# Performance work log

Measured on AMD Instinct MI355X. Metric: run time of the kernel, lower is better.

The kernel has to match this reference:

```python
import jax, jax.numpy as jnp
import numpy as np

B, S, D = 4, 2048, 512
H = 8
DK = D // H
DFF = 2048
EPS = 1e-5


def _layernorm(x, g, b):
    mu = jnp.mean(x, axis=-1, keepdims=True)
    var = jnp.mean((x - mu) ** 2, axis=-1, keepdims=True)
    return (x - mu) * jax.lax.rsqrt(var + EPS) * g + b


def setup_inputs() -> dict:
    key = jax.random.key(0)
    ks = jax.random.split(key, 12)
    s = 1.0 / np.sqrt(D)
    sf = 1.0 / np.sqrt(DFF)
    return {
        "x": jax.random.normal(ks[0], (B, S, D), dtype=jnp.float32),
        "Wq": jax.random.uniform(ks[1], (D, D), jnp.float32, -s, s),
        "bq": jnp.zeros((D,), jnp.float32),
        "Wk": jax.random.uniform(ks[2], (D, D), jnp.float32, -s, s),
        "bk": jnp.zeros((D,), jnp.float32),
        "Wv": jax.random.uniform(ks[3], (D, D), jnp.float32, -s, s),
        "bv": jnp.zeros((D,), jnp.float32),
        "Wo": jax.random.uniform(ks[4], (D, D), jnp.float32, -s, s),
        "bo": jnp.zeros((D,), jnp.float32),
        "W1": jax.random.uniform(ks[5], (D, DFF), jnp.float32, -s, s),
        "b1": jnp.zeros((DFF,), jnp.float32),
        "W2": jax.random.uniform(ks[6], (DFF, D), jnp.float32, -sf, sf),
        "b2": jnp.zeros((D,), jnp.float32),
        "g1": jnp.ones((D,), jnp.float32),
        "be1": jnp.zeros((D,), jnp.float32),
        "g2": jnp.ones((D,), jnp.float32),
        "be2": jnp.zeros((D,), jnp.float32),
    }


def reference(x, Wq, bq, Wk, bk, Wv, bv, Wo, bo, W1, b1, W2, b2, g1, be1, g2, be2):
    # Multi-head attention (dropout = identity at eval)
    def heads(v):  # [B,S,D] -> [B,H,S,DK]
        return v.reshape(B, S, H, DK).transpose(0, 2, 1, 3)

    q = heads(x @ Wq + bq)
    k = heads(x @ Wk + bk)
    v = heads(x @ Wv + bv)
    scores = jnp.einsum("bhsd,bhtd->bhst", q, k) / np.sqrt(DK)
    attn = jax.nn.softmax(scores, axis=-1)
    ctx = jnp.einsum("bhst,bhtd->bhsd", attn, v)
    ctx = ctx.transpose(0, 2, 1, 3).reshape(B, S, D)
    attn_out = ctx @ Wo + bo

    x1 = _layernorm(x + attn_out, g1, be1)

    ff = jax.nn.relu(x1 @ W1 + b1) @ W2 + b2
    return _layernorm(x1 + ff, g2, be2)
```

## Files before the change

kernel.cpp:

```cpp
#include <hip/hip_runtime.h>
#include <hip/hip_bf16.h>
#include <stdint.h>

typedef __bf16 bf16;
typedef __attribute__((ext_vector_type(8))) __bf16 bf16x8;
typedef __attribute__((ext_vector_type(4))) float f32x4;

#define DEVI __device__ __forceinline__

constexpr int Bz = 4, Sz = 2048, Dz = 512, Hz = 8, DKz = 64, DFFz = 2048;
constexpr int ROWSz = Bz * Sz;
constexpr float EPSf = 1e-5f;
constexpr float C2f = 0.125f * 1.44269504088896f;

DEVI void load_lds16(void* lds, const void* g) {
  __builtin_amdgcn_global_load_lds(
      (const __attribute__((address_space(1))) void*)(uintptr_t)(g),
      (__attribute__((address_space(3))) void*)(uint32_t)(uintptr_t)(lds),
      16, 0, 0);
}

DEVI void permswap32(unsigned& x, unsigned& y) {
  asm("v_permlane32_swap_b32 %0, %1" : "+v"(x), "+v"(y));
}
DEVI void permswap16(unsigned& x, unsigned& y) {
  asm("v_permlane16_swap_b32 %0, %1" : "+v"(x), "+v"(y));
}

template <int BM, int BK, int EPI>
__global__ __launch_bounds__(256, BM == 128 ? 4 : 3) void gemm_bt(
    const bf16* __restrict__ A, const bf16* __restrict__ Bt,
    const float* __restrict__ bias, const float* __restrict__ resid,
    const bf16* __restrict__ residb, bf16* __restrict__ aux,
    void* __restrict__ Cout, int M, int N, int K) {
  constexpr int BN = 128;
  constexpr int MI = BM / 32;
  constexpr int RPI = 512 / BK;
  constexpr int AISS = (BM / 4) / RPI;
  constexpr int BISS = 32 / RPI;
  __shared__ alignas(16) bf16 sA[2][BM * BK];
  __shared__ alignas(16) bf16 sB[2][BN * BK];
  const int tid = threadIdx.x;
  const int lane = tid & 63;
  const int wv = tid >> 6;
  const int n0 = blockIdx.x * BN;
  const int m0 = blockIdx.y * BM;

  const int srow = (BK == 32) ? (lane >> 2) : (lane >> 3);
  const int sch = (BK == 32) ? (((lane & 3) ^ (srow & 3)) * 8)
                             : (((lane & 7) ^ (srow & 7)) * 8);
  const bf16* gA = A + (size_t)(m0 + wv * (BM / 4) + srow) * K + sch;
  const bf16* gB = Bt + (size_t)(n0 + wv * 32 + srow) * K + sch;

  const int wm = (wv >> 1) * (BM / 2);
  const int wn = (wv & 1) * 64;
  const int fr = lane & 15;
  const int fq = lane >> 4;

  auto stage = [&](int buf, int k0) {
#pragma unroll
    for (int j = 0; j < AISS; ++j)
      load_lds16(sA[buf] + (wv * (BM / 4) + j * RPI) * BK, gA + (size_t)(j * RPI) * K + k0);
#pragma unroll
    for (int j = 0; j < BISS; ++j)
      load_lds16(sB[buf] + (wv * 32 + j * RPI) * BK, gB + (size_t)(j * RPI) * K + k0);
  };

  f32x4 acc[MI][4] = {};

  stage(0, 0);
  __syncthreads();

  const int niter = K / BK;
  for (int it = 0; it < niter; ++it) {
    const int cur = it & 1;
    if (it + 1 < niter) stage(cur ^ 1, (it + 1) * BK);
#pragma unroll
    for (int kk = 0; kk < BK / 32; ++kk) {
      const int fc = (BK == 32) ? ((fq ^ (fr & 3)) * 8)
                                : (((4 * kk + fq) ^ (fr & 7)) * 8);
      bf16x8 af[MI], bfr[4];
#pragma unroll
      for (int i = 0; i < MI; ++i)
        af[i] = *(const bf16x8*)(sA[cur] + (wm + i * 16 + fr) * BK + fc);
#pragma unroll
      for (int j = 0; j < 4; ++j)
        bfr[j] = *(const bf16x8*)(sB[cur] + (wn + j * 16 + fr) * BK + fc);
#pragma unroll
      for (int i = 0; i < MI; ++i)
#pragma unroll
        for (int j = 0; j < 4; ++j)
          acc[i][j] = __builtin_amdgcn_mfma_f32_16x16x32_bf16(af[i], bfr[j], acc[i][j], 0, 0, 0);
    }
    __syncthreads();
  }

#pragma unroll
  for (int i = 0; i < MI; ++i) {
#pragma unroll
    for (int j = 0; j < 4; ++j) {
      const int col = n0 + wn + j * 16 + fr;
      const float bv = bias[col];
      if (EPI == 3 && col >= 1024) {
        const int row0 = m0 + wm + i * 16 + fq * 4;
        const int hh = (col - 1024) >> 6, dk = (col - 1024) & 63;
        const int bb = row0 >> 11, s0 = row0 & 2047;
        bf16 pv[4];
#pragma unroll
        for (int r = 0; r < 4; ++r) pv[r] = (bf16)(acc[i][j][r] + bv);
        *(uint2*)(aux + (size_t)((bb * 8 + hh) * 64 + dk) * 2048 + s0) = *(const uint2*)pv;
      } else {
#pragma unroll
        for (int r = 0; r < 4; ++r) {
          const int row = m0 + wm + i * 16 + fq * 4 + r;
          const size_t idx = (size_t)row * N + col;
          float v = acc[i][j][r] + bv;
          if (EPI == 1) {
            ((bf16*)Cout)[idx] = (bf16)(v + resid[idx]);
          } else if (EPI == 2) {
            ((bf16*)Cout)[idx] = (bf16)(v > 0.f ? v : 0.f);
          } else if (EPI == 3) {
            ((bf16*)Cout)[idx] = (bf16)(col < 512 ? v * C2f : v);
          } else {
            ((bf16*)Cout)[idx] = (bf16)(v + (float)residb[idx]);
          }
        }
      }
    }
  }
}

__global__ __launch_bounds__(256, 2) void flash_attn(
    const bf16* __restrict__ qkv, const bf16* __restrict__ Vt,
    bf16* __restrict__ ctx) {
  const int bid = blockIdx.x;
  const int qt = bid & 15;
  const int h = (bid >> 4) & 7;
  const int b = bid >> 7;
  const int q0 = qt * 128;
  const int tid = threadIdx.x, lane = tid & 63, wv = tid >> 6;
  const int fr = lane & 15, fq = lane >> 4;
  const int xsw = fr & 7;

  __shared__ alignas(16) bf16 sK[3][64 * 64];
  __shared__ alignas(16) bf16 sV[3][64 * 64];

  const int srow = lane >> 3;
  const int scol = ((lane & 7) ^ srow) * 8;

  const bf16* gQ = qkv + (size_t)(b * Sz + q0 + wv * 32 + srow) * 1536 + h * 64 + scol;
  const bf16* gK = qkv + (size_t)(b * Sz + wv * 16 + srow) * 1536 + 512 + h * 64 + scol;
  const bf16* gV = Vt + (size_t)((b * 8 + h) * 64 + wv * 16 + srow) * Sz + scol;

  bf16* sQ = (bf16*)sK;
#pragma unroll
  for (int i = 0; i < 4; ++i)
    load_lds16(sQ + (wv * 32 + i * 8) * 64, gQ + (size_t)(i * 8) * 1536);
  asm volatile("s_waitcnt vmcnt(0)" ::: "memory");

  const int colc0 = (fq ^ xsw) * 8;
  const int colc1 = ((fq + 4) ^ xsw) * 8;
  int qsrc[4];
#pragma unroll
  for (int r = 0; r < 4; ++r) qsrc[r] = (fq * 4 + r) | (lane & 48);

  bf16x8 qb[2][2];
#pragma unroll
  for (int s = 0; s < 2; ++s) {
    qb[s][0] = *(const bf16x8*)(sQ + (wv * 32 + s * 16 + fr) * 64 + colc0);
    qb[s][1] = *(const bf16x8*)(sQ + (wv * 32 + s * 16 + fr) * 64 + colc1);
  }
  asm volatile("s_waitcnt lgkmcnt(0)" ::: "memory");
  __syncthreads();

  auto stage = [&](int buf, int t) {
    const size_t t0r = (size_t)t * 64;
    load_lds16(sK[buf] + (wv * 16 + 0) * 64, gK + t0r * 1536);
    load_lds16(sK[buf] + (wv * 16 + 8) * 64, gK + (t0r + 8) * 1536);
    load_lds16(sV[buf] + (wv * 16 + 0) * 64, gV + t0r);
    load_lds16(sV[buf] + (wv * 16 + 8) * 64, gV + (size_t)8 * Sz + t0r);
  };

  stage(0, 0);
  stage(1, 1);
  asm volatile("s_waitcnt vmcnt(4)" ::: "memory");
  __builtin_amdgcn_s_barrier();
  asm volatile("" ::: "memory");

  float l_part[2] = {0.f, 0.f};
  f32x4 acc_o[2][4] = {};
  int cur = 0;

  for (int it = 0; it < 32; ++it) {
    if (it + 2 < 32) {
      int nb = cur + 2;
      if (nb >= 3) nb -= 3;
      stage(nb, it + 2);
    }

    bf16x8 kf[2][4];
#pragma unroll
    for (int j = 0; j < 4; ++j) {
      kf[0][j] = *(const bf16x8*)(sK[cur] + (j * 16 + fr) * 64 + colc0);
      kf[1][j] = *(const bf16x8*)(sK[cur] + (j * 16 + fr) * 64 + colc1);
    }
    f32x4 sc[2][4] = {};
    __builtin_amdgcn_s_setprio(1);
#pragma unroll
    for (int s = 0; s < 2; ++s)
#pragma unroll
      for (int kk = 0; kk < 2; ++kk)
#pragma unroll
        for (int j = 0; j < 4; ++j)
          sc[s][j] = __builtin_amdgcn_mfma_f32_16x16x32_bf16(kf[kk][j], qb[s][kk], sc[s][j], 0, 0, 0);
    __builtin_amdgcn_s_setprio(0);

    bf16x8 pa[2][2];
#pragma unroll
    for (int s = 0; s < 2; ++s) {
      unsigned c0[4], c1[4];
      float rs = 0.f;
#pragma unroll
      for (int j = 0; j < 4; ++j) {
        float e0 = __builtin_amdgcn_exp2f(sc[s][j][0]);
        float e1 = __builtin_amdgcn_exp2f(sc[s][j][1]);
        float e2 = __builtin_amdgcn_exp2f(sc[s][j][2]);
        float e3 = __builtin_amdgcn_exp2f(sc[s][j][3]);
        rs += (e0 + e1) + (e2 + e3);
        union { bf16 hh[2]; unsigned u; } pka, pkb;
        pka.hh[0] = (bf16)e0; pka.hh[1] = (bf16)e1;
        pkb.hh[0] = (bf16)e2; pkb.hh[1] = (bf16)e3;
        c0[j] = pka.u;
        c1[j] = pkb.u;
      }
      l_part[s] += rs;
#pragma unroll
      for (int kk = 0; kk < 2; ++kk) {
        unsigned x0 = c0[2 * kk], y0 = c0[2 * kk + 1];
        permswap32(x0, y0);
        permswap16(x0, y0);
        unsigned x1 = c1[2 * kk], y1 = c1[2 * kk + 1];
        permswap32(x1, y1);
        permswap16(x1, y1);
        union { unsigned u[4]; bf16x8 v; } pk;
        pk.u[0] = x0; pk.u[1] = x1; pk.u[2] = y0; pk.u[3] = y1;
        pa[s][kk] = pk.v;
      }
    }

    bf16x8 vf[2][4];
#pragma unroll
    for (int j = 0; j < 4; ++j) {
      vf[0][j] = *(const bf16x8*)(sV[cur] + (j * 16 + fr) * 64 + colc0);
      vf[1][j] = *(const bf16x8*)(sV[cur] + (j * 16 + fr) * 64 + colc1);
    }
    __builtin_amdgcn_s_setprio(1);
#pragma unroll
    for (int s = 0; s < 2; ++s)
#pragma unroll
      for (int kk = 0; kk < 2; ++kk)
#pragma unroll
        for (int j = 0; j < 4; ++j)
          acc_o[s][j] = __builtin_amdgcn_mfma_f32_16x16x32_bf16(pa[s][kk], vf[kk][j], acc_o[s][j], 0, 0, 0);
    __builtin_amdgcn_s_setprio(0);

    if (it < 31) {
      if (it < 30) asm volatile("s_waitcnt vmcnt(4)" ::: "memory");
      else         asm volatile("s_waitcnt vmcnt(0)" ::: "memory");
      __builtin_amdgcn_s_barrier();
      asm volatile("" ::: "memory");
    }
    cur = cur == 2 ? 0 : cur + 1;
  }

#pragma unroll
  for (int s = 0; s < 2; ++s) {
    float l = l_part[s];
    l += __shfl_xor(l, 16, 64);
    l += __shfl_xor(l, 32, 64);
    float rl[4];
#pragma unroll
    for (int r = 0; r < 4; ++r) rl[r] = 1.0f / __shfl(l, qsrc[r], 64);
#pragma unroll
    for (int j = 0; j < 4; ++j)
#pragma unroll
      for (int r = 0; r < 4; ++r) {
        const int row = b * Sz + q0 + wv * 32 + s * 16 + fq * 4 + r;
        const int col = h * 64 + j * 16 + fr;
        ctx[(size_t)row * Dz + col] = (bf16)(acc_o[s][j][r] * rl[r]);
      }
  }
}

template <int OUT_F32>
__global__ __launch_bounds__(256) void layer_norm_k(
    const bf16* __restrict__ y, const float* __restrict__ g,
    const float* __restrict__ be, void* __restrict__ out) {
  const int row = blockIdx.x * 4 + (threadIdx.x >> 6);
  const int lane = threadIdx.x & 63;
  const int col = lane * 8;
  bf16x8 hv = *(const bf16x8*)(y + (size_t)row * Dz + col);
  float v[8];
  float s = 0.f, ss = 0.f;
#pragma unroll
  for (int i = 0; i < 8; ++i) {
    v[i] = (float)hv[i];
    s += v[i];
    ss += v[i] * v[i];
  }
#pragma unroll
  for (int o = 1; o < 64; o <<= 1) {
    s += __shfl_xor(s, o, 64);
    ss += __shfl_xor(ss, o, 64);
  }
  const float mu = s * (1.0f / Dz);
  const float rstd = rsqrtf(ss * (1.0f / Dz) - mu * mu + EPSf);
  const float4* g4 = (const float4*)(g + col);
  const float4* b4 = (const float4*)(be + col);
  float4 ga = g4[0], gb = g4[1], ba = b4[0], bb = b4[1];
  float o8[8];
  o8[0] = (v[0] - mu) * rstd * ga.x + ba.x;
  o8[1] = (v[1] - mu) * rstd * ga.y + ba.y;
  o8[2] = (v[2] - mu) * rstd * ga.z + ba.z;
  o8[3] = (v[3] - mu) * rstd * ga.w + ba.w;
  o8[4] = (v[4] - mu) * rstd * gb.x + bb.x;
  o8[5] = (v[5] - mu) * rstd * gb.y + bb.y;
  o8[6] = (v[6] - mu) * rstd * gb.z + bb.z;
  o8[7] = (v[7] - mu) * rstd * gb.w + bb.w;
  if (OUT_F32) {
    float4* of = (float4*)((float*)out + (size_t)row * Dz + col);
    of[0] = make_float4(o8[0], o8[1], o8[2], o8[3]);
    of[1] = make_float4(o8[4], o8[5], o8[6], o8[7]);
  } else {
    bf16 ob[8];
#pragma unroll
    for (int i = 0; i < 8; ++i) ob[i] = (bf16)o8[i];
    *(uint4*)((bf16*)out + (size_t)row * Dz + col) = *(const uint4*)ob;
  }
}

__global__ __launch_bounds__(256) void prep_all(
    const float* __restrict__ Wq, const float* __restrict__ Wk,
    const float* __restrict__ Wv, const float* __restrict__ Wo,
    const float* __restrict__ W1, const float* __restrict__ W2,
    const float* __restrict__ bq, const float* __restrict__ bk,
    const float* __restrict__ bv, const float* __restrict__ x,
    bf16* __restrict__ WqkvT, bf16* __restrict__ WoT,
    bf16* __restrict__ W1T, bf16* __restrict__ W2T,
    float* __restrict__ bqkv, bf16* __restrict__ xb) {
  __shared__ float tile[64][65];
  const int blk = blockIdx.x;
  const int t = threadIdx.x;
  if (blk < 768) {
    const float* W;
    bf16* Wt;
    int K, N, local;
    if (blk < 64)       { W = Wq; Wt = WqkvT;                       K = 512;  N = 512;  local = blk; }
    else if (blk < 128) { W = Wk; Wt = WqkvT + (size_t)512 * 512;   K = 512;  N = 512;  local = blk - 64; }
    else if (blk < 192) { W = Wv; Wt = WqkvT + (size_t)1024 * 512;  K = 512;  N = 512;  local = blk - 128; }
    else if (blk < 256) { W = Wo; Wt = WoT;                         K = 512;  N = 512;  local = blk - 192; }
    else if (blk < 512) { W = W1; Wt = W1T;                         K = 512;  N = 2048; local = blk - 256; }
    else                { W = W2; Wt = W2T;                         K = 2048; N = 512;  local = blk - 512; }
    const int kt = K / 64;
    const int k0 = (local % kt) * 64, n0 = (local / kt) * 64;
    const int r = t >> 2, c = (t & 3) * 16;
    const float* src = W + (size_t)(k0 + r) * N + n0 + c;
#pragma unroll
    for (int i = 0; i < 4; ++i) {
      float4 v = ((const float4*)src)[i];
      tile[r][c + i * 4 + 0] = v.x;
      tile[r][c + i * 4 + 1] = v.y;
      tile[r][c + i * 4 + 2] = v.z;
      tile[r][c + i * 4 + 3] = v.w;
    }
    __syncthreads();
    union { bf16 hh[16]; uint4 u[2]; } pk;
#pragma unroll
    for (int i = 0; i < 16; ++i) pk.hh[i] = (bf16)tile[c + i][r];
    uint4* dst = (uint4*)(Wt + (size_t)(n0 + r) * K + k0 + c);
    dst[0] = pk.u[0];
    dst[1] = pk.u[1];
  } else if (blk == 768) {
    for (int i = t; i < 1536; i += 256)
      bqkv[i] = i < 512 ? bq[i] : (i < 1024 ? bk[i - 512] : bv[i - 1024]);
  } else {
    const int local = blk - 769;
#pragma unroll
    for (int k = 0; k < 4; ++k) {
      const int i = local * 1024 + k * 256 + t;
      float4 v = ((const float4*)x)[i];
      bf16 tv[4] = {(bf16)v.x, (bf16)v.y, (bf16)v.z, (bf16)v.w};
      ((uint2*)xb)[i] = *(const uint2*)tv;
    }
  }
}

extern "C" void kernel_launch(void* const* d_in, const int* in_sizes, int n_in,
                              void* d_out, int out_size, void* d_ws, size_t ws_size,
                              hipStream_t stream) {
  const float* x   = (const float*)d_in[0];
  const float* Wq  = (const float*)d_in[1];
  const float* bq  = (const float*)d_in[2];
  const float* Wk  = (const float*)d_in[3];
  const float* bk  = (const float*)d_in[4];
  const float* Wv  = (const float*)d_in[5];
  const float* bvp = (const float*)d_in[6];
  const float* Wo  = (const float*)d_in[7];
  const float* bo  = (const float*)d_in[8];
  const float* W1  = (const float*)d_in[9];
  const float* b1  = (const float*)d_in[10];
  const float* W2  = (const float*)d_in[11];
  const float* b2  = (const float*)d_in[12];
  const float* g1  = (const float*)d_in[13];
  const float* be1 = (const float*)d_in[14];
  const float* g2  = (const float*)d_in[15];
  const float* be2 = (const float*)d_in[16];

  char* ws = (char*)d_ws;
  size_t off = 0;
  auto alloc = [&](size_t bytes) -> void* {
    void* p = ws + off;
    off += (bytes + 255) & ~(size_t)255;
    return p;
  };
  bf16*  WqkvT = (bf16*)alloc((size_t)1536 * 512 * 2);
  float* bqkv  = (float*)alloc(1536 * 4);
  bf16*  WoT   = (bf16*)alloc((size_t)512 * 512 * 2);
  bf16*  W1T   = (bf16*)alloc((size_t)2048 * 512 * 2);
  bf16*  W2T   = (bf16*)alloc((size_t)512 * 2048 * 2);
  bf16*  xb    = (bf16*)alloc((size_t)ROWSz * 512 * 2);
  bf16*  qkv   = (bf16*)alloc((size_t)ROWSz * 1536 * 2);
  bf16*  Vt    = (bf16*)alloc((size_t)32 * 64 * 2048 * 2);
  bf16*  ctx   = (bf16*)alloc((size_t)ROWSz * 512 * 2);
  bf16*  y1    = (bf16*)alloc((size_t)ROWSz * 512 * 2);
  bf16*  x1b   = (bf16*)alloc((size_t)ROWSz * 512 * 2);
  bf16*  hbuf  = qkv;
  bf16*  y2    = y1;

  prep_all<<<dim3(1793), 256, 0, stream>>>(Wq, Wk, Wv, Wo, W1, W2, bq, bk, bvp, x,
                                           WqkvT, WoT, W1T, W2T, bqkv, xb);

  gemm_bt<128, 32, 3><<<dim3(12, 64), 256, 0, stream>>>(xb, WqkvT, bqkv, nullptr, nullptr, Vt, qkv, ROWSz, 1536, 512);
  flash_attn<<<dim3(512), 256, 0, stream>>>(qkv, Vt, ctx);
  gemm_bt<64, 64, 4><<<dim3(4, 128), 256, 0, stream>>>(ctx, WoT, bo, nullptr, xb, nullptr, y1, ROWSz, 512, 512);
  layer_norm_k<0><<<dim3(2048), 256, 0, stream>>>(y1, g1, be1, x1b);
  gemm_bt<128, 32, 2><<<dim3(16, 64), 256, 0, stream>>>(x1b, W1T, b1, nullptr, nullptr, nullptr, hbuf, ROWSz, 2048, 512);
  gemm_bt<64, 64, 4><<<dim3(4, 128), 256, 0, stream>>>(hbuf, W2T, b2, nullptr, x1b, nullptr, y2, ROWSz, 512, 2048);
  layer_norm_k<1><<<dim3(2048), 256, 0, stream>>>(y2, g2, be2, d_out);
}
```

Measured before the change: 251.0 us.

## Software-pipeline flash attention: overlap next-tile QK^T with current softmax and PV

Moves the attention loop to a four-buffer LDS ring with three tiles prefetched ahead instead of a three-buffer ring with two. The loop is restructured so each step computes scores for tile t+1 while exponentiating and multiplying scores for tile t, ping-ponging between two score register sets. The point is to keep the matrix units busy while exp and permute work runs, and to hide more global-load latency. In exchange it raises LDS use to 64KB per block and adds register pressure from the extra score set, which could limit occupancy at two blocks per CU.

Measured after the change: 243.9 us. 2.8% less time.

```diff
diff --git a/kernel.cpp b/kernel.cpp
--- a/kernel.cpp
+++ b/kernel.cpp
@@ -142,8 +142,8 @@
   const int fr = lane & 15, fq = lane >> 4;
   const int xsw = fr & 7;
 
-  __shared__ alignas(16) bf16 sK[3][64 * 64];
-  __shared__ alignas(16) bf16 sV[3][64 * 64];
+  __shared__ alignas(16) bf16 sK[4][64 * 64];
+  __shared__ alignas(16) bf16 sV[4][64 * 64];
 
   const int srow = lane >> 3;
   const int scol = ((lane & 7) ^ srow) * 8;
@@ -183,77 +183,98 @@
 
   stage(0, 0);
   stage(1, 1);
+  stage(2, 2);
+  asm volatile("s_waitcnt vmcnt(8)" ::: "memory");
+  __builtin_amdgcn_s_barrier();
+  asm volatile("" ::: "memory");
+
+  float l_part[2] = {0.f, 0.f};
+  f32x4 acc_o[2][4] = {};
+  f32x4 scA[2][4], scB[2][4];
+
+  {
+    bf16x8 kf[2][4];
+#pragma unroll
+    for (int j = 0; j < 4; ++j) {
+      kf[0][j] = *(const bf16x8*)(sK[0] + (j * 16 + fr) * 64 + colc0);
+      kf[1][j] = *(const bf16x8*)(sK[0] + (j * 16 + fr) * 64 + colc1);
+    }
+#pragma unroll
+    for (int s = 0; s < 2; ++s)
+#pragma unroll
+      for (int j = 0; j < 4; ++j) {
+        f32x4 z = {0.f, 0.f, 0.f, 0.f};
+        z = __builtin_amdgcn_mfma_f32_16x16x32_bf16(kf[0][j], qb[s][0], z, 0, 0, 0);
+        scA[s][j] = __builtin_amdgcn_mfma_f32_16x16x32_bf16(kf[1][j], qb[s][1], z, 0, 0, 0);
+      }
+  }
   asm volatile("s_waitcnt vmcnt(4)" ::: "memory");
   __builtin_amdgcn_s_barrier();
   asm volatile("" ::: "memory");
 
-  float l_part[2] = {0.f, 0.f};
-  f32x4 acc_o[2][4] = {};
-  int cur = 0;
-
-  for (int it = 0; it < 32; ++it) {
-    if (it + 2 < 32) {
-      int nb = cur + 2;
-      if (nb >= 3) nb -= 3;
-      stage(nb, it + 2);
-    }
-
-    bf16x8 kf[2][4];
+  auto body = [&](int t, f32x4 (&scC)[2][4], f32x4 (&scN)[2][4],
+                  bool do_stage, bool do_qkt, bool wait4, bool wait0, bool do_bar) {
+    if (do_stage) stage((t + 3) & 3, t + 3);
+
+    const bf16* kb = sK[(t + 1) & 3];
+    const bf16* vb = sV[t & 3];
+    bf16x8 kf[2][4], vf[2][4];
+    if (do_qkt) {
+#pragma unroll
+      for (int j = 0; j < 4; ++j) {
+        kf[0][j] = *(const bf16x8*)(kb + (j * 16 + fr) * 64 + colc0);
+        kf[1][j] = *(const bf16x8*)(kb + (j * 16 + fr) * 64 + colc1);
+      }
+    }
 #pragma unroll
     for (int j = 0; j < 4; ++j) {
-      kf[0][j] = *(const bf16x8*)(sK[cur] + (j * 16 + fr) * 64 + colc0);
-      kf[1][j] = *(const bf16x8*)(sK[cur] + (j * 16 + fr) * 64 + colc1);
-    }
-    f32x4 sc[2][4] = {};
+      vf[0][j] = *(const bf16x8*)(vb + (j * 16 + fr) * 64 + colc0);
+      vf[1][j] = *(const bf16x8*)(vb + (j * 16 + fr) * 64 + colc1);
+    }
+
+    unsigned c0[2][4], c1[2][4];
+    float rs0 = 0.f, rs1 = 0.f;
     __builtin_amdgcn_s_setprio(1);
 #pragma unroll
+    for (int g = 0; g < 8; ++g) {
+      const int s = g >> 2, j = g & 3;
+      if (do_qkt) {
+        f32x4 z = {0.f, 0.f, 0.f, 0.f};
+        z = __builtin_amdgcn_mfma_f32_16x16x32_bf16(kf[0][j], qb[s][0], z, 0, 0, 0);
+        scN[s][j] = __builtin_amdgcn_mfma_f32_16x16x32_bf16(kf[1][j], qb[s][1], z, 0, 0, 0);
+      }
+      float e0 = __builtin_amdgcn_exp2f(scC[s][j][0]);
+      float e1 = __builtin_amdgcn_exp2f(scC[s][j][1]);
+      float e2 = __builtin_amdgcn_exp2f(scC[s][j][2]);
+      float e3 = __builtin_amdgcn_exp2f(scC[s][j][3]);
+      if (s == 0) rs0 += (e0 + e1) + (e2 + e3);
+      else        rs1 += (e0 + e1) + (e2 + e3);
+      union { bf16 hh[2]; unsigned u; } pka, pkb;
+      pka.hh[0] = (bf16)e0; pka.hh[1] = (bf16)e1;
+      pkb.hh[0] = (bf16)e2; pkb.hh[1] = (bf16)e3;
+      c0[s][j] = pka.u;
+      c1[s][j] = pkb.u;
+    }
+    __builtin_amdgcn_s_setprio(0);
+    l_part[0] += rs0;
+    l_part[1] += rs1;
+
+    bf16x8 pa[2][2];
+#pragma unroll
     for (int s = 0; s < 2; ++s)
 #pragma unroll
-      for (int kk = 0; kk < 2; ++kk)
-#pragma unroll
-        for (int j = 0; j < 4; ++j)
-          sc[s][j] = __builtin_amdgcn_mfma_f32_16x16x32_bf16(kf[kk][j], qb[s][kk], sc[s][j], 0, 0, 0);
-    __builtin_amdgcn_s_setprio(0);
-
-    bf16x8 pa[2][2];
-#pragma unroll
-    for (int s = 0; s < 2; ++s) {
-      unsigned c0[4], c1[4];
-      float rs = 0.f;
-#pragma unroll
-      for (int j = 0; j < 4; ++j) {
-        float e0 = __builtin_amdgcn_exp2f(sc[s][j][0]);
-        float e1 = __builtin_amdgcn_exp2f(sc[s][j][1]);
-        float e2 = __builtin_amdgcn_exp2f(sc[s][j][2]);
-        float e3 = __builtin_amdgcn_exp2f(sc[s][j][3]);
-        rs += (e0 + e1) + (e2 + e3);
-        union { bf16 hh[2]; unsigned u; } pka, pkb;
-        pka.hh[0] = (bf16)e0; pka.hh[1] = (bf16)e1;
-        pkb.hh[0] = (bf16)e2; pkb.hh[1] = (bf16)e3;
-        c0[j] = pka.u;
-        c1[j] = pkb.u;
-      }
-      l_part[s] += rs;
-#pragma unroll
       for (int kk = 0; kk < 2; ++kk) {
-        unsigned x0 = c0[2 * kk], y0 = c0[2 * kk + 1];
+        unsigned x0 = c0[s][2 * kk], y0 = c0[s][2 * kk + 1];
         permswap32(x0, y0);
         permswap16(x0, y0);
-        unsigned x1 = c1[2 * kk], y1 = c1[2 * kk + 1];
+        unsigned x1 = c1[s][2 * kk], y1 = c1[s][2 * kk + 1];
         permswap32(x1, y1);
         permswap16(x1, y1);
         union { unsigned u[4]; bf16x8 v; } pk;
         pk.u[0] = x0; pk.u[1] = x1; pk.u[2] = y0; pk.u[3] = y1;
         pa[s][kk] = pk.v;
       }
-    }
-
-    bf16x8 vf[2][4];
-#pragma unroll
-    for (int j = 0; j < 4; ++j) {
-      vf[0][j] = *(const bf16x8*)(sV[cur] + (j * 16 + fr) * 64 + colc0);
-      vf[1][j] = *(const bf16x8*)(sV[cur] + (j * 16 + fr) * 64 + colc1);
-    }
+
     __builtin_amdgcn_s_setprio(1);
 #pragma unroll
     for (int s = 0; s < 2; ++s)
@@ -264,14 +285,22 @@
           acc_o[s][j] = __builtin_amdgcn_mfma_f32_16x16x32_bf16(pa[s][kk], vf[kk][j], acc_o[s][j], 0, 0, 0);
     __builtin_amdgcn_s_setprio(0);
 
-    if (it < 31) {
-      if (it < 30) asm volatile("s_waitcnt vmcnt(4)" ::: "memory");
-      else         asm volatile("s_waitcnt vmcnt(0)" ::: "memory");
+    if (wait4) asm volatile("s_waitcnt vmcnt(4)" ::: "memory");
+    if (wait0) asm volatile("s_waitcnt vmcnt(0)" ::: "memory");
+    if (do_bar) {
       __builtin_amdgcn_s_barrier();
       asm volatile("" ::: "memory");
     }
-    cur = cur == 2 ? 0 : cur + 1;
-  }
+  };
+
+  for (int t = 0; t < 28; t += 2) {
+    body(t,     scA, scB, true, true, true, false, true);
+    body(t + 1, scB, scA, true, true, true, false, true);
+  }
+  body(28, scA, scB, true,  true,  true,  false, true);
+  body(29, scB, scA, false, true,  false, true,  true);
+  body(30, scA, scB, false, true,  false, false, false);
+  body(31, scB, scA, false, false, false, false, false);
 
 #pragma unroll
   for (int s = 0; s < 2; ++s) {
```

## Shrink attention query tile to 64 rows and raise occupancy with double buffering

Applied to the files above, without the earlier changes.

The flash attention kernel now gives each block 64 query rows instead of 128, with each wave owning one 16-row slice. The grid doubles to 1024 blocks, and the launch bound rises to 4 blocks per CU. K/V staging drops from a triple buffer to a double buffer to save LDS, and Q is staged through a spare V buffer. The aim is more resident waves to hide latency and a better spread of blocks across CUs. The cost is halved K/V reuse per block, which doubles K/V global traffic, plus less load/compute overlap because of the full vmcnt(0) wait each iteration.

Result: faster. 245.8 us (-2.1%).

```diff
diff --git a/kernel.cpp b/kernel.cpp
--- a/kernel.cpp
+++ b/kernel.cpp
@@ -130,48 +130,28 @@
   }
 }
 
-__global__ __launch_bounds__(256, 2) void flash_attn(
+__global__ __launch_bounds__(256, 4) void flash_attn(
     const bf16* __restrict__ qkv, const bf16* __restrict__ Vt,
     bf16* __restrict__ ctx) {
   const int bid = blockIdx.x;
-  const int qt = bid & 15;
-  const int h = (bid >> 4) & 7;
-  const int b = bid >> 7;
-  const int q0 = qt * 128;
+  const int qt = bid >> 5;
+  const int bh = bid & 31;
+  const int h = bh & 7;
+  const int b = bh >> 3;
+  const int q0 = qt * 64;
   const int tid = threadIdx.x, lane = tid & 63, wv = tid >> 6;
   const int fr = lane & 15, fq = lane >> 4;
   const int xsw = fr & 7;
 
-  __shared__ alignas(16) bf16 sK[3][64 * 64];
-  __shared__ alignas(16) bf16 sV[3][64 * 64];
+  __shared__ alignas(16) bf16 sK[2][64 * 64];
+  __shared__ alignas(16) bf16 sV[2][64 * 64];
 
   const int srow = lane >> 3;
   const int scol = ((lane & 7) ^ srow) * 8;
 
-  const bf16* gQ = qkv + (size_t)(b * Sz + q0 + wv * 32 + srow) * 1536 + h * 64 + scol;
+  const bf16* gQ = qkv + (size_t)(b * Sz + q0 + wv * 16 + srow) * 1536 + h * 64 + scol;
   const bf16* gK = qkv + (size_t)(b * Sz + wv * 16 + srow) * 1536 + 512 + h * 64 + scol;
   const bf16* gV = Vt + (size_t)((b * 8 + h) * 64 + wv * 16 + srow) * Sz + scol;
-
-  bf16* sQ = (bf16*)sK;
-#pragma unroll
-  for (int i = 0; i < 4; ++i)
-    load_lds16(sQ + (wv * 32 + i * 8) * 64, gQ + (size_t)(i * 8) * 1536);
-  asm volatile("s_waitcnt vmcnt(0)" ::: "memory");
-
-  const int colc0 = (fq ^ xsw) * 8;
-  const int colc1 = ((fq + 4) ^ xsw) * 8;
-  int qsrc[4];
-#pragma unroll
-  for (int r = 0; r < 4; ++r) qsrc[r] = (fq * 4 + r) | (lane & 48);
-
-  bf16x8 qb[2][2];
-#pragma unroll
-  for (int s = 0; s < 2; ++s) {
-    qb[s][0] = *(const bf16x8*)(sQ + (wv * 32 + s * 16 + fr) * 64 + colc0);
-    qb[s][1] = *(const bf16x8*)(sQ + (wv * 32 + s * 16 + fr) * 64 + colc1);
-  }
-  asm volatile("s_waitcnt lgkmcnt(0)" ::: "memory");
-  __syncthreads();
 
   auto stage = [&](int buf, int t) {
     const size_t t0r = (size_t)t * 64;
@@ -181,22 +161,33 @@
     load_lds16(sV[buf] + (wv * 16 + 8) * 64, gV + (size_t)8 * Sz + t0r);
   };
 
+  bf16* sQ = (bf16*)sV[1];
+  load_lds16(sQ + (wv * 16 + 0) * 64, gQ);
+  load_lds16(sQ + (wv * 16 + 8) * 64, gQ + (size_t)8 * 1536);
   stage(0, 0);
+  asm volatile("s_waitcnt vmcnt(4)" ::: "memory");
+
+  const int colc0 = (fq ^ xsw) * 8;
+  const int colc1 = ((fq + 4) ^ xsw) * 8;
+  int qsrc[4];
+#pragma unroll
+  for (int r = 0; r < 4; ++r) qsrc[r] = (fq * 4 + r) | (lane & 48);
+
+  bf16x8 qb[2];
+  qb[0] = *(const bf16x8*)(sQ + (wv * 16 + fr) * 64 + colc0);
+  qb[1] = *(const bf16x8*)(sQ + (wv * 16 + fr) * 64 + colc1);
+  asm volatile("s_waitcnt lgkmcnt(0)" ::: "memory");
   stage(1, 1);
   asm volatile("s_waitcnt vmcnt(4)" ::: "memory");
   __builtin_amdgcn_s_barrier();
   asm volatile("" ::: "memory");
 
-  float l_part[2] = {0.f, 0.f};
-  f32x4 acc_o[2][4] = {};
-  int cur = 0;
-
-  for (int it = 0; it < 32; ++it) {
-    if (it + 2 < 32) {
-      int nb = cur + 2;
-      if (nb >= 3) nb -= 3;
-      stage(nb, it + 2);
-    }
+  float l_part = 0.f;
+  f32x4 acc_o[4] = {};
+
+  for (int t = 0; t < 32; ++t) {
+    const int cur = t & 1;
+    if (t >= 1 && t + 1 < 32) stage(cur ^ 1, t + 1);
 
     bf16x8 kf[2][4];
 #pragma unroll
@@ -204,48 +195,45 @@
       kf[0][j] = *(const bf16x8*)(sK[cur] + (j * 16 + fr) * 64 + colc0);
       kf[1][j] = *(const bf16x8*)(sK[cur] + (j * 16 + fr) * 64 + colc1);
     }
-    f32x4 sc[2][4] = {};
+    f32x4 sc[4];
     __builtin_amdgcn_s_setprio(1);
 #pragma unroll
-    for (int s = 0; s < 2; ++s)
-#pragma unroll
-      for (int kk = 0; kk < 2; ++kk)
-#pragma unroll
-        for (int j = 0; j < 4; ++j)
-          sc[s][j] = __builtin_amdgcn_mfma_f32_16x16x32_bf16(kf[kk][j], qb[s][kk], sc[s][j], 0, 0, 0);
+    for (int j = 0; j < 4; ++j) {
+      f32x4 z = {0.f, 0.f, 0.f, 0.f};
+      z = __builtin_amdgcn_mfma_f32_16x16x32_bf16(kf[0][j], qb[0], z, 0, 0, 0);
+      sc[j] = __builtin_amdgcn_mfma_f32_16x16x32_bf16(kf[1][j], qb[1], z, 0, 0, 0);
+    }
     __builtin_amdgcn_s_setprio(0);
 
-    bf16x8 pa[2][2];
-#pragma unroll
-    for (int s = 0; s < 2; ++s) {
-      unsigned c0[4], c1[4];
-      float rs = 0.f;
-#pragma unroll
-      for (int j = 0; j < 4; ++j) {
-        float e0 = __builtin_amdgcn_exp2f(sc[s][j][0]);
-        float e1 = __builtin_amdgcn_exp2f(sc[s][j][1]);
-        float e2 = __builtin_amdgcn_exp2f(sc[s][j][2]);
-        float e3 = __builtin_amdgcn_exp2f(sc[s][j][3]);
-        rs += (e0 + e1) + (e2 + e3);
-        union { bf16 hh[2]; unsigned u; } pka, pkb;
-        pka.hh[0] = (bf16)e0; pka.hh[1] = (bf16)e1;
-        pkb.hh[0] = (bf16)e2; pkb.hh[1] = (bf16)e3;
-        c0[j] = pka.u;
-        c1[j] = pkb.u;
-      }
-      l_part[s] += rs;
-#pragma unroll
-      for (int kk = 0; kk < 2; ++kk) {
-        unsigned x0 = c0[2 * kk], y0 = c0[2 * kk + 1];
-        permswap32(x0, y0);
-        permswap16(x0, y0);
-        unsigned x1 = c1[2 * kk], y1 = c1[2 * kk + 1];
-        permswap32(x1, y1);
-        permswap16(x1, y1);
-        union { unsigned u[4]; bf16x8 v; } pk;
-        pk.u[0] = x0; pk.u[1] = x1; pk.u[2] = y0; pk.u[3] = y1;
-        pa[s][kk] = pk.v;
-      }
+    unsigned c0[4], c1[4];
+    float rs = 0.f;
+#pragma unroll
+    for (int j = 0; j < 4; ++j) {
+      float e0 = __builtin_amdgcn_exp2f(sc[j][0]);
+      float e1 = __builtin_amdgcn_exp2f(sc[j][1]);
+      float e2 = __builtin_amdgcn_exp2f(sc[j][2]);
+      float e3 = __builtin_amdgcn_exp2f(sc[j][3]);
+      rs += (e0 + e1) + (e2 + e3);
+      union { bf16 hh[2]; unsigned u; } pka, pkb;
+      pka.hh[0] = (bf16)e0; pka.hh[1] = (bf16)e1;
+      pkb.hh[0] = (bf16)e2; pkb.hh[1] = (bf16)e3;
+      c0[j] = pka.u;
+      c1[j] = pkb.u;
+    }
+    l_part += rs;
+
+    bf16x8 pa[2];
+#pragma unroll
+    for (int kk = 0; kk < 2; ++kk) {
+      unsigned x0 = c0[2 * kk], y0 = c0[2 * kk + 1];
+      permswap32(x0, y0);
+      permswap16(x0, y0);
+      unsigned x1 = c1[2 * kk], y1 = c1[2 * kk + 1];
+      permswap32(x1, y1);
+      permswap16(x1, y1);
+      union { unsigned u[4]; bf16x8 v; } pk;
+      pk.u[0] = x0; pk.u[1] = x1; pk.u[2] = y0; pk.u[3] = y1;
+      pa[kk] = pk.v;
     }
 
     bf16x8 vf[2][4];
@@ -256,40 +244,33 @@
     }
     __builtin_amdgcn_s_setprio(1);
 #pragma unroll
-    for (int s = 0; s < 2; ++s)
-#pragma unroll
-      for (int kk = 0; kk < 2; ++kk)
-#pragma unroll
-        for (int j = 0; j < 4; ++j)
-          acc_o[s][j] = __builtin_amdgcn_mfma_f32_16x16x32_bf16(pa[s][kk], vf[kk][j], acc_o[s][j], 0, 0, 0);
+    for (int kk = 0; kk < 2; ++kk)
+#pragma unroll
+      for (int j = 0; j < 4; ++j)
+        acc_o[j] = __builtin_amdgcn_mfma_f32_16x16x32_bf16(pa[kk], vf[kk][j], acc_o[j], 0, 0, 0);
     __builtin_amdgcn_s_setprio(0);
 
-    if (it < 31) {
-      if (it < 30) asm volatile("s_waitcnt vmcnt(4)" ::: "memory");
-      else         asm volatile("s_waitcnt vmcnt(0)" ::: "memory");
+    if (t + 1 < 32) {
+      asm volatile("s_waitcnt vmcnt(0)" ::: "memory");
       __builtin_amdgcn_s_barrier();
       asm volatile("" ::: "memory");
     }
-    cur = cur == 2 ? 0 : cur + 1;
-  }
-
-#pragma unroll
-  for (int s = 0; s < 2; ++s) {
-    float l = l_part[s];
-    l += __shfl_xor(l, 16, 64);
-    l += __shfl_xor(l, 32, 64);
-    float rl[4];
-#pragma unroll
-    for (int r = 0; r < 4; ++r) rl[r] = 1.0f / __shfl(l, qsrc[r], 64);
-#pragma unroll
-    for (int j = 0; j < 4; ++j)
-#pragma unroll
-      for (int r = 0; r < 4; ++r) {
-        const int row = b * Sz + q0 + wv * 32 + s * 16 + fq * 4 + r;
-        const int col = h * 64 + j * 16 + fr;
-        ctx[(size_t)row * Dz + col] = (bf16)(acc_o[s][j][r] * rl[r]);
-      }
-  }
+  }
+
+  float l = l_part;
+  l += __shfl_xor(l, 16, 64);
+  l += __shfl_xor(l, 32, 64);
+  float rl[4];
+#pragma unroll
+  for (int r = 0; r < 4; ++r) rl[r] = 1.0f / __shfl(l, qsrc[r], 64);
+#pragma unroll
+  for (int j = 0; j < 4; ++j)
+#pragma unroll
+    for (int r = 0; r < 4; ++r) {
+      const int row = b * Sz + q0 + wv * 16 + fq * 4 + r;
+      const int col = h * 64 + j * 16 + fr;
+      ctx[(size_t)row * Dz + col] = (bf16)(acc_o[j][r] * rl[r]);
+    }
 }
 
 template <int OUT_F32>
@@ -441,7 +422,7 @@
                                            WqkvT, WoT, W1T, W2T, bqkv, xb);
 
   gemm_bt<128, 32, 3><<<dim3(12, 64), 256, 0, stream>>>(xb, WqkvT, bqkv, nullptr, nullptr, Vt, qkv, ROWSz, 1536, 512);
-  flash_attn<<<dim3(512), 256, 0, stream>>>(qkv, Vt, ctx);
+  flash_attn<<<dim3(1024), 256, 0, stream>>>(qkv, Vt, ctx);
   gemm_bt<64, 64, 4><<<dim3(4, 128), 256, 0, stream>>>(ctx, WoT, bo, nullptr, xb, nullptr, y1, ROWSz, 512, 512);
   layer_norm_k<0><<<dim3(2048), 256, 0, stream>>>(y1, g1, be1, x1b);
   gemm_bt<128, 32, 2><<<dim3(16, 64), 256, 0, stream>>>(x1b, W1T, b1, nullptr, nullptr, nullptr, hbuf, ROWSz, 2048, 512);
```

## Split attention KV range across two wave groups and merge partial results in LDS

Applied to the files above, without the earlier changes.

The flash attention kernel grows from 256 to 512 threads. Two groups of four waves each process half of the key/value sequence with double-buffered LDS staging, and their partial outputs and row sums are merged through a shared-memory union at the end. Q is now loaded straight from global into registers instead of going through LDS, and the block index order is changed so consecutive blocks cover different batch/head pairs. This doubles the waves working per query tile, aiming to hide latency better. The cost is an extra LDS merge and barrier, simpler double buffering in place of triple buffering with a full vmcnt(0) wait each step, and higher register and LDS pressure.

Result: no change. 247.0 us (-1.6%).

```diff
diff --git a/kernel.cpp b/kernel.cpp
--- a/kernel.cpp
+++ b/kernel.cpp
@@ -130,33 +130,52 @@
   }
 }
 
-__global__ __launch_bounds__(256, 2) void flash_attn(
+__global__ __launch_bounds__(512, 4) void flash_attn(
     const bf16* __restrict__ qkv, const bf16* __restrict__ Vt,
     bf16* __restrict__ ctx) {
   const int bid = blockIdx.x;
-  const int qt = bid & 15;
-  const int h = (bid >> 4) & 7;
-  const int b = bid >> 7;
+  const int qt = bid >> 5;
+  const int bh = bid & 31;
+  const int h = bh & 7;
+  const int b = bh >> 3;
   const int q0 = qt * 128;
   const int tid = threadIdx.x, lane = tid & 63, wv = tid >> 6;
+  const int g = wv >> 2;
+  const int wg = wv & 3;
   const int fr = lane & 15, fq = lane >> 4;
   const int xsw = fr & 7;
 
-  __shared__ alignas(16) bf16 sK[3][64 * 64];
-  __shared__ alignas(16) bf16 sV[3][64 * 64];
+  __shared__ alignas(16) union SMem {
+    struct { bf16 K[2][2][64 * 64]; bf16 V[2][2][64 * 64]; } kv;
+    float mrg[4 * 64 * 35];
+  } sm;
 
   const int srow = lane >> 3;
   const int scol = ((lane & 7) ^ srow) * 8;
 
-  const bf16* gQ = qkv + (size_t)(b * Sz + q0 + wv * 32 + srow) * 1536 + h * 64 + scol;
-  const bf16* gK = qkv + (size_t)(b * Sz + wv * 16 + srow) * 1536 + 512 + h * 64 + scol;
-  const bf16* gV = Vt + (size_t)((b * 8 + h) * 64 + wv * 16 + srow) * Sz + scol;
-
-  bf16* sQ = (bf16*)sK;
-#pragma unroll
-  for (int i = 0; i < 4; ++i)
-    load_lds16(sQ + (wv * 32 + i * 8) * 64, gQ + (size_t)(i * 8) * 1536);
+  const bf16* gK = qkv + (size_t)(b * Sz + wg * 16 + srow) * 1536 + 512 + h * 64 + scol;
+  const bf16* gV = Vt + (size_t)((b * 8 + h) * 64 + wg * 16 + srow) * Sz + scol;
+
+  auto stage = [&](int p, int t) {
+    const size_t t0 = (size_t)t * 64;
+    load_lds16(sm.kv.K[g][p] + (wg * 16 + 0) * 64, gK + t0 * 1536);
+    load_lds16(sm.kv.K[g][p] + (wg * 16 + 8) * 64, gK + (t0 + 8) * 1536);
+    load_lds16(sm.kv.V[g][p] + (wg * 16 + 0) * 64, gV + t0);
+    load_lds16(sm.kv.V[g][p] + (wg * 16 + 8) * 64, gV + (size_t)8 * Sz + t0);
+  };
+
+  stage(0, g * 16);
+
+  const bf16* gQf = qkv + (size_t)(b * Sz + q0 + wg * 32 + fr) * 1536 + h * 64;
+  bf16x8 qb[2][2];
+  qb[0][0] = *(const bf16x8*)(gQf + fq * 8);
+  qb[0][1] = *(const bf16x8*)(gQf + (fq + 4) * 8);
+  qb[1][0] = *(const bf16x8*)(gQf + (size_t)16 * 1536 + fq * 8);
+  qb[1][1] = *(const bf16x8*)(gQf + (size_t)16 * 1536 + (fq + 4) * 8);
+
   asm volatile("s_waitcnt vmcnt(0)" ::: "memory");
+  __builtin_amdgcn_s_barrier();
+  asm volatile("" ::: "memory");
 
   const int colc0 = (fq ^ xsw) * 8;
   const int colc1 = ((fq + 4) ^ xsw) * 8;
@@ -164,55 +183,32 @@
 #pragma unroll
   for (int r = 0; r < 4; ++r) qsrc[r] = (fq * 4 + r) | (lane & 48);
 
-  bf16x8 qb[2][2];
-#pragma unroll
-  for (int s = 0; s < 2; ++s) {
-    qb[s][0] = *(const bf16x8*)(sQ + (wv * 32 + s * 16 + fr) * 64 + colc0);
-    qb[s][1] = *(const bf16x8*)(sQ + (wv * 32 + s * 16 + fr) * 64 + colc1);
-  }
-  asm volatile("s_waitcnt lgkmcnt(0)" ::: "memory");
-  __syncthreads();
-
-  auto stage = [&](int buf, int t) {
-    const size_t t0r = (size_t)t * 64;
-    load_lds16(sK[buf] + (wv * 16 + 0) * 64, gK + t0r * 1536);
-    load_lds16(sK[buf] + (wv * 16 + 8) * 64, gK + (t0r + 8) * 1536);
-    load_lds16(sV[buf] + (wv * 16 + 0) * 64, gV + t0r);
-    load_lds16(sV[buf] + (wv * 16 + 8) * 64, gV + (size_t)8 * Sz + t0r);
-  };
-
-  stage(0, 0);
-  stage(1, 1);
-  asm volatile("s_waitcnt vmcnt(4)" ::: "memory");
-  __builtin_amdgcn_s_barrier();
-  asm volatile("" ::: "memory");
-
+  const f32x4 ZERO = {0.f, 0.f, 0.f, 0.f};
   float l_part[2] = {0.f, 0.f};
   f32x4 acc_o[2][4] = {};
-  int cur = 0;
-
-  for (int it = 0; it < 32; ++it) {
-    if (it + 2 < 32) {
-      int nb = cur + 2;
-      if (nb >= 3) nb -= 3;
-      stage(nb, it + 2);
-    }
+
+  for (int st = 0; st < 16; ++st) {
+    const int p = st & 1;
+    if (st + 1 < 16) stage(p ^ 1, g * 16 + st + 1);
+
+    const bf16* kb = sm.kv.K[g][p];
+    const bf16* vb = sm.kv.V[g][p];
 
     bf16x8 kf[2][4];
 #pragma unroll
     for (int j = 0; j < 4; ++j) {
-      kf[0][j] = *(const bf16x8*)(sK[cur] + (j * 16 + fr) * 64 + colc0);
-      kf[1][j] = *(const bf16x8*)(sK[cur] + (j * 16 + fr) * 64 + colc1);
-    }
-    f32x4 sc[2][4] = {};
+      kf[0][j] = *(const bf16x8*)(kb + (j * 16 + fr) * 64 + colc0);
+      kf[1][j] = *(const bf16x8*)(kb + (j * 16 + fr) * 64 + colc1);
+    }
+    f32x4 sc[2][4];
     __builtin_amdgcn_s_setprio(1);
 #pragma unroll
     for (int s = 0; s < 2; ++s)
 #pragma unroll
-      for (int kk = 0; kk < 2; ++kk)
-#pragma unroll
-        for (int j = 0; j < 4; ++j)
-          sc[s][j] = __builtin_amdgcn_mfma_f32_16x16x32_bf16(kf[kk][j], qb[s][kk], sc[s][j], 0, 0, 0);
+      for (int j = 0; j < 4; ++j) {
+        f32x4 z = __builtin_amdgcn_mfma_f32_16x16x32_bf16(kf[0][j], qb[s][0], ZERO, 0, 0, 0);
+        sc[s][j] = __builtin_amdgcn_mfma_f32_16x16x32_bf16(kf[1][j], qb[s][1], z, 0, 0, 0);
+      }
     __builtin_amdgcn_s_setprio(0);
 
     bf16x8 pa[2][2];
@@ -251,8 +247,8 @@
     bf16x8 vf[2][4];
 #pragma unroll
     for (int j = 0; j < 4; ++j) {
-      vf[0][j] = *(const bf16x8*)(sV[cur] + (j * 16 + fr) * 64 + colc0);
-      vf[1][j] = *(const bf16x8*)(sV[cur] + (j * 16 + fr) * 64 + colc1);
+      vf[0][j] = *(const bf16x8*)(vb + (j * 16 + fr) * 64 + colc0);
+      vf[1][j] = *(const bf16x8*)(vb + (j * 16 + fr) * 64 + colc1);
     }
     __builtin_amdgcn_s_setprio(1);
 #pragma unroll
@@ -264,31 +260,54 @@
           acc_o[s][j] = __builtin_amdgcn_mfma_f32_16x16x32_bf16(pa[s][kk], vf[kk][j], acc_o[s][j], 0, 0, 0);
     __builtin_amdgcn_s_setprio(0);
 
-    if (it < 31) {
-      if (it < 30) asm volatile("s_waitcnt vmcnt(4)" ::: "memory");
-      else         asm volatile("s_waitcnt vmcnt(0)" ::: "memory");
+    if (st + 1 < 16) {
+      asm volatile("s_waitcnt vmcnt(0)" ::: "memory");
       __builtin_amdgcn_s_barrier();
       asm volatile("" ::: "memory");
     }
-    cur = cur == 2 ? 0 : cur + 1;
-  }
-
-#pragma unroll
-  for (int s = 0; s < 2; ++s) {
-    float l = l_part[s];
-    l += __shfl_xor(l, 16, 64);
-    l += __shfl_xor(l, 32, 64);
-    float rl[4];
-#pragma unroll
-    for (int r = 0; r < 4; ++r) rl[r] = 1.0f / __shfl(l, qsrc[r], 64);
-#pragma unroll
-    for (int j = 0; j < 4; ++j)
-#pragma unroll
-      for (int r = 0; r < 4; ++r) {
-        const int row = b * Sz + q0 + wv * 32 + s * 16 + fq * 4 + r;
-        const int col = h * 64 + j * 16 + fr;
-        ctx[(size_t)row * Dz + col] = (bf16)(acc_o[s][j][r] * rl[r]);
-      }
+  }
+
+  __syncthreads();
+  if (g == 0) {
+    float* mp = sm.mrg + (wg * 64 + lane) * 35;
+#pragma unroll
+    for (int s = 0; s < 2; ++s)
+#pragma unroll
+      for (int j = 0; j < 4; ++j)
+#pragma unroll
+        for (int r = 0; r < 4; ++r) mp[s * 16 + j * 4 + r] = acc_o[s][j][r];
+    mp[32] = l_part[0];
+    mp[33] = l_part[1];
+  }
+  __syncthreads();
+  if (g == 1) {
+    const float* mp = sm.mrg + (wg * 64 + lane) * 35;
+#pragma unroll
+    for (int s = 0; s < 2; ++s)
+#pragma unroll
+      for (int j = 0; j < 4; ++j)
+#pragma unroll
+        for (int r = 0; r < 4; ++r) acc_o[s][j][r] += mp[s * 16 + j * 4 + r];
+    l_part[0] += mp[32];
+    l_part[1] += mp[33];
+
+#pragma unroll
+    for (int s = 0; s < 2; ++s) {
+      float l = l_part[s];
+      l += __shfl_xor(l, 16, 64);
+      l += __shfl_xor(l, 32, 64);
+      float rl[4];
+#pragma unroll
+      for (int r = 0; r < 4; ++r) rl[r] = 1.0f / __shfl(l, qsrc[r], 64);
+#pragma unroll
+      for (int j = 0; j < 4; ++j)
+#pragma unroll
+        for (int r = 0; r < 4; ++r) {
+          const int row = b * Sz + q0 + wg * 32 + s * 16 + fq * 4 + r;
+          const int col = h * 64 + j * 16 + fr;
+          ctx[(size_t)row * Dz + col] = (bf16)(acc_o[s][j][r] * rl[r]);
+        }
+    }
   }
 }
 
@@ -441,7 +460,7 @@
                                            WqkvT, WoT, W1T, W2T, bqkv, xb);
 
   gemm_bt<128, 32, 3><<<dim3(12, 64), 256, 0, stream>>>(xb, WqkvT, bqkv, nullptr, nullptr, Vt, qkv, ROWSz, 1536, 512);
-  flash_attn<<<dim3(512), 256, 0, stream>>>(qkv, Vt, ctx);
+  flash_attn<<<dim3(512), 512, 0, stream>>>(qkv, Vt, ctx);
   gemm_bt<64, 64, 4><<<dim3(4, 128), 256, 0, stream>>>(ctx, WoT, bo, nullptr, xb, nullptr, y1, ROWSz, 512, 512);
   layer_norm_k<0><<<dim3(2048), 256, 0, stream>>>(y1, g1, be1, x1b);
   gemm_bt<128, 32, 2><<<dim3(16, 64), 256, 0, stream>>>(x1b, W1T, b1, nullptr, nullptr, nullptr, hbuf, ROWSz, 2048, 512);
```
